# Kernel tuning notes

Measured on AMD Instinct MI355X. Metric: run time of the kernel, lower is better.

Reference implementation:

```python
import jax, jax.numpy as jnp
import numpy as np

POOL = 7        # output pooled size
SAMP = 2 * POOL # crop_and_resize sampling resolution (14)


def _bilinear_crop(feat, ys, xs):
    """feat [H,W,C]; ys,xs [N,S] sample coords in feature-map pixels -> [N,S,S,C]."""
    H, W, _ = feat.shape
    ys = jnp.clip(ys, 0.0, H - 1.0)
    xs = jnp.clip(xs, 0.0, W - 1.0)
    y0f = jnp.floor(ys); x0f = jnp.floor(xs)
    y0 = y0f.astype(jnp.int32); x0 = x0f.astype(jnp.int32)
    y1 = jnp.clip(y0 + 1, 0, H - 1); x1 = jnp.clip(x0 + 1, 0, W - 1)
    wy = (ys - y0f)[:, :, None, None]   # [N,S,1,1]
    wx = (xs - x0f)[:, None, :, None]   # [N,1,S,1]
    g = lambda yi, xi: feat[yi[:, :, None], xi[:, None, :]]  # [N,S,S,C]
    out = g(y0, x0) * (1 - wy) * (1 - wx)
    out = out + g(y0, x1) * (1 - wy) * wx
    out = out + g(y1, x0) * wy * (1 - wx)
    out = out + g(y1, x1) * wy * wx
    return out


def setup_inputs() -> dict:
    key = jax.random.key(0)
    k1, k2, k3, k4, k5 = jax.random.split(key, 5)
    Hf, Wf, C = 37, 50, 512
    N = 1000
    H_img, W_img = 600.0, 800.0
    inputs = jax.random.normal(k1, (1, Hf, Wf, C), dtype=jnp.float32)
    # random valid boxes (x1,y1,x2,y2) in image coords
    cx = jax.random.uniform(k2, (N,)) * W_img
    cy = jax.random.uniform(k3, (N,)) * H_img
    bw = jax.random.uniform(k4, (N,)) * 300.0 + 16.0
    bh = jax.random.uniform(k5, (N,)) * 300.0 + 16.0
    x1 = jnp.clip(cx - bw / 2, 0.0, W_img - 1.0)
    y1 = jnp.clip(cy - bh / 2, 0.0, H_img - 1.0)
    x2 = jnp.clip(cx + bw / 2, 0.0, W_img - 1.0)
    y2 = jnp.clip(cy + bh / 2, 0.0, H_img - 1.0)
    rois = jnp.stack([x1, y1, x2, y2], axis=1).astype(jnp.float32)
    im_size = jnp.array([600, 800], dtype=jnp.int32)  # (h, w)
    return {"inputs": inputs, "rois": rois, "im_size": im_size}


def reference(inputs, rois, im_size):
    feat = inputs[0]                       # [Hf, Wf, C]
    Hf, Wf, C = feat.shape
    h = im_size[0].astype(jnp.float32)
    w = im_size[1].astype(jnp.float32)
    # normalize boxes to [0,1] (y1, x1, y2, x2), as in roi_pool_tf
    ny1 = rois[:, 1] / h; nx1 = rois[:, 0] / w
    ny2 = rois[:, 3] / h; nx2 = rois[:, 2] / w
    # crop_and_resize sample grid (TF convention: endpoints at box corners)
    t = jnp.linspace(0.0, 1.0, SAMP, dtype=jnp.float32)          # [S]
    ys = (ny1[:, None] + (ny2 - ny1)[:, None] * t[None, :]) * (Hf - 1)  # [N,S]
    xs = (nx1[:, None] + (nx2 - nx1)[:, None] * t[None, :]) * (Wf - 1)  # [N,S]
    crops = _bilinear_crop(feat, ys, xs)   # [N,14,14,C]
    N = crops.shape[0]
    pooled = crops.reshape(N, POOL, 2, POOL, 2, C).max(axis=(2, 4))  # [N,7,7,C]
    return pooled
```

## Files before the change

kernel.cpp:

```cpp
#include <hip/hip_runtime.h>
#include <math.h>

#define HF 37
#define WF 50
#define CC 512
#define POOLD 7
#define SAMPD 14

__global__ __launch_bounds__(128) void roipool_kernel(
    const float* __restrict__ feat,
    const float* __restrict__ rois,
    const int*   __restrict__ im_size,
    float*       __restrict__ out,
    int N)
{
    int bid = blockIdx.x;
    int n   = bid / (POOLD * POOLD);
    if (n >= N) return;
    int rem = bid - n * (POOLD * POOLD);
    int py  = rem / POOLD;
    int px  = rem - py * POOLD;

    float h = (float)im_size[0];
    float w = (float)im_size[1];
    float bx1 = rois[4 * n + 0];
    float by1 = rois[4 * n + 1];
    float bx2 = rois[4 * n + 2];
    float by2 = rois[4 * n + 3];
    float ny1 = by1 / h, nx1 = bx1 / w;
    float ny2 = by2 / h, nx2 = bx2 / w;

    const float inv = 1.0f / (float)(SAMPD - 1);

    int c = (int)threadIdx.x * 4;

    float4 acc = make_float4(-INFINITY, -INFINITY, -INFINITY, -INFINITY);

    #pragma unroll
    for (int dy = 0; dy < 2; ++dy) {
        int sy = 2 * py + dy;
        float ty = (float)sy * inv;
        float ys = (ny1 + (ny2 - ny1) * ty) * (float)(HF - 1);
        ys = fminf(fmaxf(ys, 0.0f), (float)(HF - 1));
        float y0f = floorf(ys);
        int iy0 = (int)y0f;
        int iy1 = min(iy0 + 1, HF - 1);
        float wy = ys - y0f;

        #pragma unroll
        for (int dx = 0; dx < 2; ++dx) {
            int sx = 2 * px + dx;
            float tx = (float)sx * inv;
            float xs = (nx1 + (nx2 - nx1) * tx) * (float)(WF - 1);
            xs = fminf(fmaxf(xs, 0.0f), (float)(WF - 1));
            float x0f = floorf(xs);
            int ix0 = (int)x0f;
            int ix1 = min(ix0 + 1, WF - 1);
            float wx = xs - x0f;

            const float4* p00 = (const float4*)(feat + ((size_t)(iy0 * WF + ix0) * CC + c));
            const float4* p01 = (const float4*)(feat + ((size_t)(iy0 * WF + ix1) * CC + c));
            const float4* p10 = (const float4*)(feat + ((size_t)(iy1 * WF + ix0) * CC + c));
            const float4* p11 = (const float4*)(feat + ((size_t)(iy1 * WF + ix1) * CC + c));
            float4 v00 = *p00;
            float4 v01 = *p01;
            float4 v10 = *p10;
            float4 v11 = *p11;

            float w00 = (1.0f - wy) * (1.0f - wx);
            float w01 = (1.0f - wy) * wx;
            float w10 = wy * (1.0f - wx);
            float w11 = wy * wx;

            float4 val;
            val.x = v00.x * w00 + v01.x * w01 + v10.x * w10 + v11.x * w11;
            val.y = v00.y * w00 + v01.y * w01 + v10.y * w10 + v11.y * w11;
            val.z = v00.z * w00 + v01.z * w01 + v10.z * w10 + v11.z * w11;
            val.w = v00.w * w00 + v01.w * w01 + v10.w * w10 + v11.w * w11;

            acc.x = fmaxf(acc.x, val.x);
            acc.y = fmaxf(acc.y, val.y);
            acc.z = fmaxf(acc.z, val.z);
            acc.w = fmaxf(acc.w, val.w);
        }
    }

    float4* dst = (float4*)(out + ((size_t)((n * POOLD + py) * POOLD + px) * CC + c));
    *dst = acc;
}

extern "C" void kernel_launch(void* const* d_in, const int* in_sizes, int n_in,
                              void* d_out, int out_size, void* d_ws, size_t ws_size,
                              hipStream_t stream) {
    const float* feat    = (const float*)d_in[0];
    const float* rois    = (const float*)d_in[1];
    const int*   im_size = (const int*)d_in[2];
    float* out = (float*)d_out;

    int N = in_sizes[1] / 4;
    int nblocks = N * POOLD * POOLD;
    roipool_kernel<<<nblocks, 128, 0, stream>>>(feat, rois, im_size, out, N);
}
```

Before: 146.9 us.

## Process a full pooled row per block and reuse adjacent column samples

Each block now handles one pooled row (all 7 px bins) rather than a single bin. It sweeps the 14 x sample positions and keeps the previously loaded columns in registers, so feature loads are reused when consecutive samples share a source column. Bilinear interpolation is rewritten as separable lerps, and row and column indices are made wave-uniform with readfirstlane. This cuts redundant global or L2 loads and per-block overhead, at the cost of 7x fewer blocks, more registers per thread and data-dependent branches.

```diff
diff --git a/kernel.cpp b/kernel.cpp
--- a/kernel.cpp
+++ b/kernel.cpp
@@ -7,6 +7,24 @@
 #define POOLD 7
 #define SAMPD 14
 
+__device__ __forceinline__ float4 lerp4(float4 a, float4 b, float t) {
+    float4 r;
+    r.x = a.x + t * (b.x - a.x);
+    r.y = a.y + t * (b.y - a.y);
+    r.z = a.z + t * (b.z - a.z);
+    r.w = a.w + t * (b.w - a.w);
+    return r;
+}
+
+__device__ __forceinline__ float4 max4(float4 a, float4 b) {
+    float4 r;
+    r.x = fmaxf(a.x, b.x);
+    r.y = fmaxf(a.y, b.y);
+    r.z = fmaxf(a.z, b.z);
+    r.w = fmaxf(a.w, b.w);
+    return r;
+}
+
 __global__ __launch_bounds__(128) void roipool_kernel(
     const float* __restrict__ feat,
     const float* __restrict__ rois,
@@ -15,11 +33,9 @@
     int N)
 {
     int bid = blockIdx.x;
-    int n   = bid / (POOLD * POOLD);
+    int n   = bid / POOLD;
+    int py  = bid - n * POOLD;
     if (n >= N) return;
-    int rem = bid - n * (POOLD * POOLD);
-    int py  = rem / POOLD;
-    int px  = rem - py * POOLD;
 
     float h = (float)im_size[0];
     float w = (float)im_size[1];
@@ -32,61 +48,96 @@
 
     const float inv = 1.0f / (float)(SAMPD - 1);
 
-    int c = (int)threadIdx.x * 4;
-
-    float4 acc = make_float4(-INFINITY, -INFINITY, -INFINITY, -INFINITY);
-
-    #pragma unroll
-    for (int dy = 0; dy < 2; ++dy) {
-        int sy = 2 * py + dy;
-        float ty = (float)sy * inv;
+    float wya, wyb;
+    int rowoff[4];
+    {
+        float ty = (float)(2 * py) * inv;
         float ys = (ny1 + (ny2 - ny1) * ty) * (float)(HF - 1);
         ys = fminf(fmaxf(ys, 0.0f), (float)(HF - 1));
         float y0f = floorf(ys);
         int iy0 = (int)y0f;
         int iy1 = min(iy0 + 1, HF - 1);
-        float wy = ys - y0f;
+        wya = ys - y0f;
+        rowoff[0] = __builtin_amdgcn_readfirstlane(iy0) * (WF * CC);
+        rowoff[1] = __builtin_amdgcn_readfirstlane(iy1) * (WF * CC);
 
-        #pragma unroll
-        for (int dx = 0; dx < 2; ++dx) {
-            int sx = 2 * px + dx;
-            float tx = (float)sx * inv;
-            float xs = (nx1 + (nx2 - nx1) * tx) * (float)(WF - 1);
-            xs = fminf(fmaxf(xs, 0.0f), (float)(WF - 1));
-            float x0f = floorf(xs);
-            int ix0 = (int)x0f;
-            int ix1 = min(ix0 + 1, WF - 1);
-            float wx = xs - x0f;
-
-            const float4* p00 = (const float4*)(feat + ((size_t)(iy0 * WF + ix0) * CC + c));
-            const float4* p01 = (const float4*)(feat + ((size_t)(iy0 * WF + ix1) * CC + c));
-            const float4* p10 = (const float4*)(feat + ((size_t)(iy1 * WF + ix0) * CC + c));
-            const float4* p11 = (const float4*)(feat + ((size_t)(iy1 * WF + ix1) * CC + c));
-            float4 v00 = *p00;
-            float4 v01 = *p01;
-            float4 v10 = *p10;
-            float4 v11 = *p11;
-
-            float w00 = (1.0f - wy) * (1.0f - wx);
-            float w01 = (1.0f - wy) * wx;
-            float w10 = wy * (1.0f - wx);
-            float w11 = wy * wx;
-
-            float4 val;
-            val.x = v00.x * w00 + v01.x * w01 + v10.x * w10 + v11.x * w11;
-            val.y = v00.y * w00 + v01.y * w01 + v10.y * w10 + v11.y * w11;
-            val.z = v00.z * w00 + v01.z * w01 + v10.z * w10 + v11.z * w11;
-            val.w = v00.w * w00 + v01.w * w01 + v10.w * w10 + v11.w * w11;
-
-            acc.x = fmaxf(acc.x, val.x);
-            acc.y = fmaxf(acc.y, val.y);
-            acc.z = fmaxf(acc.z, val.z);
-            acc.w = fmaxf(acc.w, val.w);
-        }
+        ty = (float)(2 * py + 1) * inv;
+        ys = (ny1 + (ny2 - ny1) * ty) * (float)(HF - 1);
+        ys = fminf(fmaxf(ys, 0.0f), (float)(HF - 1));
+        y0f = floorf(ys);
+        iy0 = (int)y0f;
+        iy1 = min(iy0 + 1, HF - 1);
+        wyb = ys - y0f;
+        rowoff[2] = __builtin_amdgcn_readfirstlane(iy0) * (WF * CC);
+        rowoff[3] = __builtin_amdgcn_readfirstlane(iy1) * (WF * CC);
     }
 
-    float4* dst = (float4*)(out + ((size_t)((n * POOLD + py) * POOLD + px) * CC + c));
-    *dst = acc;
+    const float* pbase = feat + (size_t)threadIdx.x * 4;
+
+    float4 acc[POOLD];
+    #pragma unroll
+    for (int i = 0; i < POOLD; ++i)
+        acc[i] = make_float4(-INFINITY, -INFINITY, -INFINITY, -INFINITY);
+
+    int ca_ix = -1, cb_ix = -1;
+    float4 colA[4], colB[4];
+
+    #pragma unroll
+    for (int sx = 0; sx < SAMPD; ++sx) {
+        float tx = (float)sx * inv;
+        float xs = (nx1 + (nx2 - nx1) * tx) * (float)(WF - 1);
+        xs = fminf(fmaxf(xs, 0.0f), (float)(WF - 1));
+        float x0f = floorf(xs);
+        int ix0 = __builtin_amdgcn_readfirstlane((int)x0f);
+        int ix1 = __builtin_amdgcn_readfirstlane(min(ix0 + 1, WF - 1));
+        float wx = xs - x0f;
+
+        float4 a[4], b[4];
+
+        if (ix0 == ca_ix) {
+            #pragma unroll
+            for (int r = 0; r < 4; ++r) a[r] = colA[r];
+        } else if (ix0 == cb_ix) {
+            #pragma unroll
+            for (int r = 0; r < 4; ++r) a[r] = colB[r];
+        } else {
+            #pragma unroll
+            for (int r = 0; r < 4; ++r)
+                a[r] = *(const float4*)(pbase + rowoff[r] + ix0 * CC);
+        }
+
+        if (ix1 == ix0) {
+            #pragma unroll
+            for (int r = 0; r < 4; ++r) b[r] = a[r];
+        } else if (ix1 == cb_ix) {
+            #pragma unroll
+            for (int r = 0; r < 4; ++r) b[r] = colB[r];
+        } else {
+            #pragma unroll
+            for (int r = 0; r < 4; ++r)
+                b[r] = *(const float4*)(pbase + rowoff[r] + ix1 * CC);
+        }
+
+        ca_ix = ix0; cb_ix = ix1;
+        #pragma unroll
+        for (int r = 0; r < 4; ++r) { colA[r] = a[r]; colB[r] = b[r]; }
+
+        float4 h0 = lerp4(a[0], b[0], wx);
+        float4 h1 = lerp4(a[1], b[1], wx);
+        float4 h2 = lerp4(a[2], b[2], wx);
+        float4 h3 = lerp4(a[3], b[3], wx);
+
+        float4 va = lerp4(h0, h1, wya);
+        float4 vb = lerp4(h2, h3, wyb);
+
+        int px = sx >> 1;
+        acc[px] = max4(acc[px], max4(va, vb));
+    }
+
+    float* obase = out + ((size_t)(n * POOLD + py) * POOLD) * CC + (size_t)threadIdx.x * 4;
+    #pragma unroll
+    for (int px = 0; px < POOLD; ++px)
+        *(float4*)(obase + (size_t)px * CC) = acc[px];
 }
 
 extern "C" void kernel_launch(void* const* d_in, const int* in_sizes, int n_in,
@@ -98,6 +149,6 @@
     float* out = (float*)d_out;
 
     int N = in_sizes[1] / 4;
-    int nblocks = N * POOLD * POOLD;
+    int nblocks = N * POOLD;
     roipool_kernel<<<nblocks, 128, 0, stream>>>(feat, rois, im_size, out, N);
 }
```

New measurement: 187.3 us. 1.27x slower.
